# Kernel tuning notes

Measured on AMD Instinct MI355X. Metric: run time of the kernel, lower is better.

Reference implementation:

```python
import jax, jax.numpy as jnp
import numpy as np

N, H, F = 1024, 4, 32       # nodes, heads, out features per head
DIN, DE = 128, 32           # node in-features, edge in-features
EPS = 1e-5                  # BatchNorm eps
SLOPE = 0.2                 # LeakyReLU negative slope


def setup_inputs() -> dict:
    key = jax.random.key(0)
    ks = jax.random.split(key, 12)
    x = jax.random.normal(ks[0], (N, DIN), jnp.float32)
    e = jax.random.normal(ks[1], (N, N, DE), jnp.float32)
    conn = jnp.where(jax.random.uniform(ks[2], (N, N)) < 0.05, 0.0, -1e9).astype(jnp.float32)
    s = 0.05
    return {
        "in_nodes_features": x,
        "in_edges_features": e,
        "connectivity_mask": conn,
        "W_proj": jax.random.normal(ks[3], (DIN, H * F), jnp.float32) * s,
        "W_edge": jax.random.normal(ks[4], (DE, H * F), jnp.float32) * s,
        "b_edge": jnp.zeros((H * F,), jnp.float32),
        "a_src": jax.random.normal(ks[5], (H, F), jnp.float32) * s,
        "a_tgt": jax.random.normal(ks[6], (H, F), jnp.float32) * s,
        "a_edge": jax.random.normal(ks[7], (H, F), jnp.float32) * s,
        "W_skip": jax.random.normal(ks[8], (DIN, H * F), jnp.float32) * s,
        "gamma": jnp.ones((H * F,), jnp.float32),
        "beta": jnp.zeros((H * F,), jnp.float32),
        "bias": jnp.zeros((H * F,), jnp.float32),
    }


def reference(in_nodes_features, in_edges_features, connectivity_mask,
              W_proj, W_edge, b_edge, a_src, a_tgt, a_edge,
              W_skip, gamma, beta, bias):
    x, e, conn = in_nodes_features, in_edges_features, connectivity_mask
    # linear projections (dropout is identity in eval mode)
    nproj = (x @ W_proj).reshape(N, H, F)                                   # [N,H,F]
    eproj = jax.nn.leaky_relu((e @ W_edge + b_edge).reshape(N, N, H, F), SLOPE)  # [N,N,H,F]
    # per-head attention logits
    s_src = jnp.einsum('ihf,hf->ih', nproj, a_src)                          # [N,H]
    s_tgt = jnp.einsum('ihf,hf->ih', nproj, a_tgt)                          # [N,H]
    s_edge = jnp.einsum('ijhf,hf->ijh', eproj, a_edge)                      # [N,N,H]
    scores = jax.nn.leaky_relu(s_src[:, None, :] + s_tgt[None, :, :] + s_edge, SLOPE)
    scores = scores + conn[:, :, None]                                      # mask non-edges
    attn = jax.nn.softmax(scores, axis=1)                                   # softmax over neighbors j
    out = jnp.einsum('ijh,jhf->ihf', attn, nproj)                           # [N,H,F] aggregation
    # skip connection (F != DIN so skip_proj path)
    out = out + (x @ W_skip).reshape(N, H, F)
    out = out.reshape(N, H * F)                                             # concat heads
    # BatchNorm1d with track_running_stats=False -> batch statistics
    mu = jnp.mean(out, axis=0)
    var = jnp.var(out, axis=0)
    out = (out - mu) / jnp.sqrt(var + EPS) * gamma + beta
    out = out + bias
    return jax.nn.elu(out)
```

## Files before the change

### kernel.cpp

```cpp
#include <hip/hip_runtime.h>
#include <cstddef>

#define NN 1024
#define HF 128
#define DE_ 32
#define SLOPE 0.2f
#define EPSV 1e-5f

__global__ __launch_bounds__(256) void proj_kernel(
    const float* __restrict__ x, const float* __restrict__ W_proj,
    const float* __restrict__ W_skip, const float* __restrict__ a_src,
    const float* __restrict__ a_tgt, float* __restrict__ nproj,
    float* __restrict__ skip, float* __restrict__ s_src,
    float* __restrict__ s_tgt)
{
  const int i = blockIdx.x, t = threadIdx.x;
  __shared__ float xs[128];
  if (t < 128) xs[t] = x[(size_t)i * 128 + t];
  __syncthreads();
  const float* W = (t < 128) ? W_proj : W_skip;
  const int c = t & 127;
  float acc = 0.f;
#pragma unroll 16
  for (int k = 0; k < 128; ++k) acc = fmaf(xs[k], W[k * 128 + c], acc);
  if (t < 128) nproj[(size_t)i * 128 + c] = acc;
  else         skip[(size_t)i * 128 + c] = acc;
  float vs = 0.f, vt = 0.f;
  if (t < 128) { vs = acc * a_src[c]; vt = acc * a_tgt[c]; }
#pragma unroll
  for (int off = 16; off; off >>= 1) {
    vs += __shfl_down(vs, off, 32);
    vt += __shfl_down(vt, off, 32);
  }
  if (t < 128 && (t & 31) == 0) {
    s_src[i * 4 + (t >> 5)] = vs;
    s_tgt[i * 4 + (t >> 5)] = vt;
  }
}

__global__ __launch_bounds__(256) void attn_kernel(
    const float* __restrict__ e,
    const float* __restrict__ conn,
    const float* __restrict__ W_edge,
    const float* __restrict__ b_edge,
    const float* __restrict__ a_edge,
    const float* __restrict__ s_src,
    const float* __restrict__ s_tgt,
    const float* __restrict__ nproj,
    const float* __restrict__ skip,
    float* __restrict__ out_pre)
{
  const int i = blockIdx.x, t = threadIdx.x;
  __shared__ unsigned short nbr[NN];
  __shared__ float sc[NN * 4];
  __shared__ float partial[256];
  __shared__ int cnt;

  const int c = t & 127;
  const int h = c >> 5;
  const int half = t >> 7;

  float Wc[DE_];
#pragma unroll
  for (int k = 0; k < DE_; ++k) Wc[k] = W_edge[k * 128 + c];
  const float aec = a_edge[c];
  const float bec = b_edge[c];
  const float ssi = s_src[i * 4 + h];

  if (t == 0) cnt = 0;
  __syncthreads();
  for (int j = t; j < NN; j += 256) {
    if (conn[(size_t)i * NN + j] > -0.5f) {
      int p = atomicAdd(&cnt, 1);
      nbr[p] = (unsigned short)j;
    }
  }
  __syncthreads();
  const int M = cnt;

  for (int n = half; n < M; n += 2) {
    const int j = nbr[n];
    const float4* ev4 = (const float4*)(e + ((size_t)i << 15) + ((size_t)j << 5));
    float acc = bec;
#pragma unroll
    for (int q = 0; q < 8; ++q) {
      float4 v = ev4[q];
      acc = fmaf(v.x, Wc[4 * q + 0], acc);
      acc = fmaf(v.y, Wc[4 * q + 1], acc);
      acc = fmaf(v.z, Wc[4 * q + 2], acc);
      acc = fmaf(v.w, Wc[4 * q + 3], acc);
    }
    acc = acc > 0.f ? acc : SLOPE * acc;
    float contrib = acc * aec;
#pragma unroll
    for (int off = 16; off; off >>= 1) contrib += __shfl_down(contrib, off, 32);
    if ((c & 31) == 0) {
      float sco = ssi + s_tgt[(size_t)j * 4 + h] + contrib;
      sco = sco > 0.f ? sco : SLOPE * sco;
      sc[n * 4 + h] = sco;
    }
  }
  __syncthreads();

  {
    const int hh = t >> 6;
    const int lane = t & 63;
    float m = -1e30f;
    for (int n = lane; n < M; n += 64) m = fmaxf(m, sc[n * 4 + hh]);
#pragma unroll
    for (int off = 32; off; off >>= 1) m = fmaxf(m, __shfl_down(m, off, 64));
    m = __shfl(m, 0, 64);
    float s = 0.f;
    for (int n = lane; n < M; n += 64) s += __expf(sc[n * 4 + hh] - m);
#pragma unroll
    for (int off = 32; off; off >>= 1) s += __shfl_down(s, off, 64);
    s = __shfl(s, 0, 64);
    const float inv = 1.f / s;
    for (int n = lane; n < M; n += 64)
      sc[n * 4 + hh] = __expf(sc[n * 4 + hh] - m) * inv;
  }
  __syncthreads();

  float accum = 0.f;
  for (int n = half; n < M; n += 2) {
    const int j = nbr[n];
    accum = fmaf(sc[n * 4 + h], nproj[(size_t)j * 128 + c], accum);
  }
  partial[t] = accum;
  __syncthreads();
  if (t < 128) {
    float tot = partial[t] + partial[t + 128] + skip[(size_t)i * 128 + t];
    out_pre[(size_t)i * 128 + t] = tot;
  }
}

__global__ __launch_bounds__(256) void bn_kernel(
    const float* __restrict__ out_pre, const float* __restrict__ gamma,
    const float* __restrict__ beta, const float* __restrict__ bias,
    float* __restrict__ out)
{
  const int c = blockIdx.x, t = threadIdx.x;
  float vals[4];
  float s = 0.f, s2 = 0.f;
#pragma unroll
  for (int q = 0; q < 4; ++q) {
    float v = out_pre[(size_t)(t + q * 256) * 128 + c];
    vals[q] = v;
    s += v;
    s2 += v * v;
  }
  __shared__ float rs[4], rs2[4], stat[2];
#pragma unroll
  for (int off = 32; off; off >>= 1) {
    s += __shfl_down(s, off, 64);
    s2 += __shfl_down(s2, off, 64);
  }
  if ((t & 63) == 0) { rs[t >> 6] = s; rs2[t >> 6] = s2; }
  __syncthreads();
  if (t == 0) {
    float S = rs[0] + rs[1] + rs[2] + rs[3];
    float S2 = rs2[0] + rs2[1] + rs2[2] + rs2[3];
    float mu = S * (1.f / 1024.f);
    float var = S2 * (1.f / 1024.f) - mu * mu;
    stat[0] = mu;
    stat[1] = rsqrtf(var + EPSV);
  }
  __syncthreads();
  const float mu = stat[0], rstd = stat[1];
  const float g = gamma[c] * rstd;
  const float b = beta[c] + bias[c] - mu * g;
#pragma unroll
  for (int q = 0; q < 4; ++q) {
    float y = vals[q] * g + b;
    out[(size_t)(t + q * 256) * 128 + c] = y > 0.f ? y : expm1f(y);
  }
}

extern "C" void kernel_launch(void* const* d_in, const int* in_sizes, int n_in,
                              void* d_out, int out_size, void* d_ws,
                              size_t ws_size, hipStream_t stream)
{
  const float* x      = (const float*)d_in[0];
  const float* e      = (const float*)d_in[1];
  const float* conn   = (const float*)d_in[2];
  const float* W_proj = (const float*)d_in[3];
  const float* W_edge = (const float*)d_in[4];
  const float* b_edge = (const float*)d_in[5];
  const float* a_src  = (const float*)d_in[6];
  const float* a_tgt  = (const float*)d_in[7];
  const float* a_edge = (const float*)d_in[8];
  const float* W_skip = (const float*)d_in[9];
  const float* gamma  = (const float*)d_in[10];
  const float* beta   = (const float*)d_in[11];
  const float* bias   = (const float*)d_in[12];

  float* nproj   = (float*)d_ws;
  float* skip    = nproj + (size_t)NN * HF;
  float* out_pre = skip + (size_t)NN * HF;
  float* s_src   = out_pre + (size_t)NN * HF;
  float* s_tgt   = s_src + (size_t)NN * 4;

  proj_kernel<<<NN, 256, 0, stream>>>(x, W_proj, W_skip, a_src, a_tgt,
                                      nproj, skip, s_src, s_tgt);
  attn_kernel<<<NN, 256, 0, stream>>>(e, conn, W_edge, b_edge, a_edge,
                                      s_src, s_tgt, nproj, skip, out_pre);
  bn_kernel<<<HF, 256, 0, stream>>>(out_pre, gamma, beta, bias, (float*)d_out);
}
```

Baseline: 257.6 us.

## Stage edge features in shared memory and process four nodes per proj block

```diff
diff --git a/kernel.cpp b/kernel.cpp
--- a/kernel.cpp
+++ b/kernel.cpp
@@ -6,6 +6,7 @@
 #define DE_ 32
 #define SLOPE 0.2f
 #define EPSV 1e-5f
+#define ETILE 64
 
 __global__ __launch_bounds__(256) void proj_kernel(
     const float* __restrict__ x, const float* __restrict__ W_proj,
@@ -14,27 +15,45 @@
     float* __restrict__ skip, float* __restrict__ s_src,
     float* __restrict__ s_tgt)
 {
-  const int i = blockIdx.x, t = threadIdx.x;
-  __shared__ float xs[128];
-  if (t < 128) xs[t] = x[(size_t)i * 128 + t];
-  __syncthreads();
-  const float* W = (t < 128) ? W_proj : W_skip;
+  const int b = blockIdx.x, t = threadIdx.x;
+  __shared__ float xs[4 * 128];
+  xs[t] = x[(size_t)b * 512 + t];
+  xs[t + 256] = x[(size_t)b * 512 + t + 256];
+  __syncthreads();
+  const int sel = t >> 7;
+  const float* W = sel ? W_skip : W_proj;
   const int c = t & 127;
-  float acc = 0.f;
-#pragma unroll 16
-  for (int k = 0; k < 128; ++k) acc = fmaf(xs[k], W[k * 128 + c], acc);
-  if (t < 128) nproj[(size_t)i * 128 + c] = acc;
-  else         skip[(size_t)i * 128 + c] = acc;
-  float vs = 0.f, vt = 0.f;
-  if (t < 128) { vs = acc * a_src[c]; vt = acc * a_tgt[c]; }
-#pragma unroll
-  for (int off = 16; off; off >>= 1) {
-    vs += __shfl_down(vs, off, 32);
-    vt += __shfl_down(vt, off, 32);
-  }
-  if (t < 128 && (t & 31) == 0) {
-    s_src[i * 4 + (t >> 5)] = vs;
-    s_tgt[i * 4 + (t >> 5)] = vt;
+  float acc0 = 0.f, acc1 = 0.f, acc2 = 0.f, acc3 = 0.f;
+#pragma unroll 8
+  for (int k = 0; k < 128; ++k) {
+    const float w = W[k * 128 + c];
+    acc0 = fmaf(xs[k], w, acc0);
+    acc1 = fmaf(xs[128 + k], w, acc1);
+    acc2 = fmaf(xs[256 + k], w, acc2);
+    acc3 = fmaf(xs[384 + k], w, acc3);
+  }
+  float* dst = sel ? skip : nproj;
+  dst[(size_t)(4 * b + 0) * 128 + c] = acc0;
+  dst[(size_t)(4 * b + 1) * 128 + c] = acc1;
+  dst[(size_t)(4 * b + 2) * 128 + c] = acc2;
+  dst[(size_t)(4 * b + 3) * 128 + c] = acc3;
+  if (sel == 0) {
+    const float as = a_src[c], at = a_tgt[c];
+    const int h = c >> 5;
+    float accs[4] = {acc0, acc1, acc2, acc3};
+#pragma unroll
+    for (int n = 0; n < 4; ++n) {
+      float vs = accs[n] * as, vt = accs[n] * at;
+#pragma unroll
+      for (int off = 16; off; off >>= 1) {
+        vs += __shfl_down(vs, off, 32);
+        vt += __shfl_down(vt, off, 32);
+      }
+      if ((c & 31) == 0) {
+        s_src[(4 * b + n) * 4 + h] = vs;
+        s_tgt[(4 * b + n) * 4 + h] = vt;
+      }
+    }
   }
 }
 
@@ -53,6 +72,7 @@
   const int i = blockIdx.x, t = threadIdx.x;
   __shared__ unsigned short nbr[NN];
   __shared__ float sc[NN * 4];
+  __shared__ float ebuf[ETILE * 32];
   __shared__ float partial[256];
   __shared__ int cnt;
 
@@ -78,29 +98,39 @@
   __syncthreads();
   const int M = cnt;
 
-  for (int n = half; n < M; n += 2) {
-    const int j = nbr[n];
-    const float4* ev4 = (const float4*)(e + ((size_t)i << 15) + ((size_t)j << 5));
-    float acc = bec;
-#pragma unroll
-    for (int q = 0; q < 8; ++q) {
-      float4 v = ev4[q];
-      acc = fmaf(v.x, Wc[4 * q + 0], acc);
-      acc = fmaf(v.y, Wc[4 * q + 1], acc);
-      acc = fmaf(v.z, Wc[4 * q + 2], acc);
-      acc = fmaf(v.w, Wc[4 * q + 3], acc);
-    }
-    acc = acc > 0.f ? acc : SLOPE * acc;
-    float contrib = acc * aec;
-#pragma unroll
-    for (int off = 16; off; off >>= 1) contrib += __shfl_down(contrib, off, 32);
-    if ((c & 31) == 0) {
-      float sco = ssi + s_tgt[(size_t)j * 4 + h] + contrib;
-      sco = sco > 0.f ? sco : SLOPE * sco;
-      sc[n * 4 + h] = sco;
-    }
-  }
-  __syncthreads();
+  for (int base = 0; base < M; base += ETILE) {
+    const int mT = min(ETILE, M - base);
+    for (int q = t; q < mT * 8; q += 256) {
+      const int n = q >> 3, part = q & 7;
+      const int j = nbr[base + n];
+      ((float4*)ebuf)[q] =
+          ((const float4*)(e + ((size_t)i << 15) + ((size_t)j << 5)))[part];
+    }
+    __syncthreads();
+    for (int n = half; n < mT; n += 2) {
+      const float4* eb4 = (const float4*)(ebuf + n * 32);
+      float acc = bec;
+#pragma unroll
+      for (int q = 0; q < 8; ++q) {
+        float4 v = eb4[q];
+        acc = fmaf(v.x, Wc[4 * q + 0], acc);
+        acc = fmaf(v.y, Wc[4 * q + 1], acc);
+        acc = fmaf(v.z, Wc[4 * q + 2], acc);
+        acc = fmaf(v.w, Wc[4 * q + 3], acc);
+      }
+      acc = acc > 0.f ? acc : SLOPE * acc;
+      float contrib = acc * aec;
+#pragma unroll
+      for (int off = 16; off; off >>= 1) contrib += __shfl_down(contrib, off, 32);
+      if ((c & 31) == 0) {
+        const int j = nbr[base + n];
+        float sco = ssi + s_tgt[(size_t)j * 4 + h] + contrib;
+        sco = sco > 0.f ? sco : SLOPE * sco;
+        sc[(base + n) * 4 + h] = sco;
+      }
+    }
+    __syncthreads();
+  }
 
   {
     const int hh = t >> 6;
@@ -200,8 +230,8 @@
   float* s_src   = out_pre + (size_t)NN * HF;
   float* s_tgt   = s_src + (size_t)NN * 4;
 
-  proj_kernel<<<NN, 256, 0, stream>>>(x, W_proj, W_skip, a_src, a_tgt,
-                                      nproj, skip, s_src, s_tgt);
+  proj_kernel<<<NN / 4, 256, 0, stream>>>(x, W_proj, W_skip, a_src, a_tgt,
+                                          nproj, skip, s_src, s_tgt);
   attn_kernel<<<NN, 256, 0, stream>>>(e, conn, W_edge, b_edge, a_edge,
                                       s_src, s_tgt, nproj, skip, out_pre);
   bn_kernel<<<HF, 256, 0, stream>>>(out_pre, gamma, beta, bias, (float*)d_out);
```

Result: faster. 230.8 us (-10.4%).
